# Optimization experiments

Measured on AMD Instinct MI355X. Metric: run time of the kernel, lower is better.

Reference implementation:

```python
import jax, jax.numpy as jnp
import numpy as np

B, T, C = 2, 2048, 1024
NH = 16
DFF = 4096
EPS = 1e-5


def setup_inputs() -> dict:
    key = jax.random.key(0)
    ks = jax.random.split(key, 12)
    s = 0.02
    return {
        "x": jax.random.normal(ks[0], (B, T, C), dtype=jnp.float32),
        "Wq": jax.random.normal(ks[1], (C, C), dtype=jnp.float32) * s,
        "bq": jax.random.normal(ks[2], (C,), dtype=jnp.float32) * s,
        "Wk": jax.random.normal(ks[3], (C, C), dtype=jnp.float32) * s,
        "bk": jax.random.normal(ks[4], (C,), dtype=jnp.float32) * s,
        "Wv": jax.random.normal(ks[5], (C, C), dtype=jnp.float32) * s,
        "bv": jax.random.normal(ks[6], (C,), dtype=jnp.float32) * s,
        "W1": jax.random.normal(ks[7], (C, DFF), dtype=jnp.float32) * s,
        "b1": jax.random.normal(ks[8], (DFF,), dtype=jnp.float32) * s,
        "W2": jax.random.normal(ks[9], (DFF, C), dtype=jnp.float32) * s,
        "b2": jax.random.normal(ks[10], (C,), dtype=jnp.float32) * s,
        "ln_w": jnp.ones((C,), dtype=jnp.float32),
    }


def _layernorm(x, w):
    # LayerNorm over last dim, weight only (bias=False), eps=1e-5
    mu = jnp.mean(x, axis=-1, keepdims=True)
    var = jnp.mean(jnp.square(x - mu), axis=-1, keepdims=True)
    return (x - mu) / jnp.sqrt(var + EPS) * w


def reference(x, Wq, bq, Wk, bk, Wv, bv, W1, b1, W2, b2, ln_w):
    Bx, Tx, Cx = x.shape
    hd = Cx // NH
    q = (x @ Wq + bq).reshape(Bx, Tx, NH, hd).transpose(0, 2, 1, 3)  # [B,H,T,hd]
    k = (x @ Wk + bk).reshape(Bx, Tx, NH, hd).transpose(0, 2, 1, 3)
    v = (x @ Wv + bv).reshape(Bx, Tx, NH, hd).transpose(0, 2, 1, 3)
    # NOTE: original scales by sqrt(d_k) = sqrt(FULL model dim C), not head dim
    scores = jnp.einsum("bhqd,bhkd->bhqk", q, k) / jnp.sqrt(jnp.float32(Cx))
    causal = jnp.tril(jnp.ones((Tx, Tx), dtype=bool))
    scores = jnp.where(causal[None, None, :, :], scores, -jnp.inf)
    attn = jax.nn.softmax(scores, axis=-1)
    head_out = jnp.einsum("bhqk,bhkd->bhqd", attn, v)
    a = head_out.transpose(0, 2, 1, 3).reshape(Bx, Tx, Cx)
    # residuals: out = x + ln(x) with SHARED ln weight
    h = a + _layernorm(a, ln_w)
    f = jax.nn.relu(h @ W1 + b1) @ W2 + b2
    out = f + _layernorm(f, ln_w)
    return out
```

## Files before the change

### kernel.cpp

```cpp
#include <hip/hip_runtime.h>
#include <math.h>


typedef __attribute__((ext_vector_type(8))) short short8;
typedef __attribute__((ext_vector_type(4))) float f32x4;

__device__ __forceinline__ unsigned short f2bf(float f) {
    unsigned u = __builtin_bit_cast(unsigned, f);
    unsigned r = u + 0x7fffu + ((u >> 16) & 1u);
    return (unsigned short)(r >> 16);
}

__global__ __launch_bounds__(256) void prep_kernel(
    const float* __restrict__ x,  const float* __restrict__ Wq,
    const float* __restrict__ Wk, const float* __restrict__ Wv,
    const float* __restrict__ W1, const float* __restrict__ W2,
    const float* __restrict__ bq, const float* __restrict__ bk,
    unsigned short* __restrict__ x_bf,  unsigned short* __restrict__ Wqk_t,
    unsigned short* __restrict__ Wvt,   unsigned short* __restrict__ W1t,
    unsigned short* __restrict__ W2t,   float* __restrict__ bqk)
{
    const int bid = blockIdx.x;
    const int tid = threadIdx.x;

    if (bid < 4096) {
        const int i = (bid * 256 + tid) * 4;
        float4 v = *(const float4*)(x + i);
        ushort4 o;
        o.x = f2bf(v.x); o.y = f2bf(v.y); o.z = f2bf(v.z); o.w = f2bf(v.w);
        *(ushort4*)(x_bf + i) = o;
        return;
    }
    if (bid >= 15360) {
        const int i = (bid - 15360) * 256 + tid;
        bqk[i] = i < 1024 ? bq[i] : bk[i - 1024];
        return;
    }

    __shared__ float tile[32][33];
    const float* src; unsigned short* dst; int K, N, t;
    if (bid < 5120)       { t = bid - 4096;  src = Wq; dst = Wqk_t;            K = 1024; N = 1024; }
    else if (bid < 6144)  { t = bid - 5120;  src = Wk; dst = Wqk_t + 1048576;  K = 1024; N = 1024; }
    else if (bid < 7168)  { t = bid - 6144;  src = Wv; dst = Wvt;              K = 1024; N = 1024; }
    else if (bid < 11264) { t = bid - 7168;  src = W1; dst = W1t;              K = 1024; N = 4096; }
    else                  { t = bid - 11264; src = W2; dst = W2t;              K = 4096; N = 1024; }

    const int ncols = N >> 5;
    const int n0 = (t % ncols) * 32;
    const int k0 = (t / ncols) * 32;
    const int tx = tid & 31;
    const int ty = tid >> 5;
#pragma unroll
    for (int i = 0; i < 4; ++i)
        tile[ty + i * 8][tx] = src[(size_t)(k0 + ty + i * 8) * N + n0 + tx];
    __syncthreads();
#pragma unroll
    for (int i = 0; i < 4; ++i)
        dst[(size_t)(n0 + ty + i * 8) * K + k0 + tx] = f2bf(tile[tx][ty + i * 8]);
}

template <int TM, int TN>
__device__ __forceinline__ void gemm_body(
    unsigned short* As, unsigned short* Bs,
    const unsigned short* __restrict__ A, const unsigned short* __restrict__ Bt,
    const float* __restrict__ bias, float* __restrict__ Cf,
    unsigned short* __restrict__ Cb, int M, int N, int K, int mode,
    int bx, int by)
{
    constexpr int NI   = TM / 32;
    constexpr int NJ   = TN / 32;
    constexpr int NPA  = TM / 8;
    constexpr int NPB  = TN / 8;
    constexpr int MAXA = (NPA + 3) / 4;
    constexpr int MAXB = (NPB + 3) / 4;

    const int tid  = threadIdx.x;
    const int lane = tid & 63;
    const int w    = tid >> 6;
    const int wm   = (w & 1) * (TM / 2);
    const int wn   = (w >> 1) * (TN / 2);
    const int fm   = lane & 15;
    const int quad = lane >> 4;

    const int row0 = by * TM;
    const int col0 = bx * TN;

    const int srow = lane >> 3;
    const int scol = ((lane & 7) ^ srow) << 3;

    const unsigned short* aptr[MAXA];
    int aoff[MAXA];
#pragma unroll
    for (int i = 0; i < MAXA; ++i) {
        const int p = w + i * 4;
        if (p < NPA) {
            aptr[i] = A + (size_t)(row0 + p * 8 + srow) * K + scol;
            aoff[i] = p * 8 * 64;
        }
    }
    const unsigned short* bptr[MAXB];
    int boff[MAXB];
#pragma unroll
    for (int i = 0; i < MAXB; ++i) {
        const int p = w + i * 4;
        if (p < NPB) {
            bptr[i] = Bt + (size_t)(col0 + p * 8 + srow) * K + scol;
            boff[i] = p * 8 * 64;
        }
    }

    f32x4 acc[NI][NJ] = {};

    for (int k0 = 0; k0 < K; k0 += 64) {
        __syncthreads();
#pragma unroll
        for (int i = 0; i < MAXA; ++i)
            if (w + i * 4 < NPA)
                __builtin_amdgcn_global_load_lds(
                    (const __attribute__((address_space(1))) void*)(aptr[i] + k0),
                    (__attribute__((address_space(3))) void*)&As[aoff[i]], 16, 0, 0);
#pragma unroll
        for (int i = 0; i < MAXB; ++i)
            if (w + i * 4 < NPB)
                __builtin_amdgcn_global_load_lds(
                    (const __attribute__((address_space(1))) void*)(bptr[i] + k0),
                    (__attribute__((address_space(3))) void*)&Bs[boff[i]], 16, 0, 0);
        __syncthreads();

#pragma unroll
        for (int kh = 0; kh < 2; ++kh) {
            short8 af[NI], bf[NJ];
#pragma unroll
            for (int i = 0; i < NI; ++i) {
                const int r = wm + i * 16 + fm;
                const int sl = ((kh << 2) | quad) ^ (r & 7);
                af[i] = *(const short8*)&As[r * 64 + sl * 8];
            }
#pragma unroll
            for (int j = 0; j < NJ; ++j) {
                const int r = wn + j * 16 + fm;
                const int sl = ((kh << 2) | quad) ^ (r & 7);
                bf[j] = *(const short8*)&Bs[r * 64 + sl * 8];
            }
#pragma unroll
            for (int i = 0; i < NI; ++i)
#pragma unroll
                for (int j = 0; j < NJ; ++j)
                    acc[i][j] = __builtin_amdgcn_mfma_f32_16x16x32_bf16(
                        af[i], bf[j], acc[i][j], 0, 0, 0);
        }
    }

#pragma unroll
    for (int j = 0; j < NJ; ++j) {
        const int col = col0 + wn + j * 16 + fm;
        const float bcol = (mode == 3) ? 0.f : bias[col];
#pragma unroll
        for (int i = 0; i < NI; ++i) {
            const int rbase = row0 + wm + i * 16 + quad * 4;
#pragma unroll
            for (int r = 0; r < 4; ++r) {
                const int row = rbase + r;
                float val = acc[i][j][r] + ((mode == 3) ? bias[row] : bcol);
                if (mode == 1) val = fmaxf(val, 0.f);
                if (mode == 0) Cf[(size_t)row * N + col] = val;
                else           Cb[(size_t)row * N + col] = f2bf(val);
            }
        }
    }
}

template <int TM, int TN>
__global__ __launch_bounds__(256) void gemm_bf16_mfma(
    const unsigned short* __restrict__ A, const unsigned short* __restrict__ Bt,
    const float* __restrict__ bias, float* __restrict__ Cf,
    unsigned short* __restrict__ Cb, int M, int N, int K, int mode)
{
    __shared__ unsigned short As[TM * 64];
    __shared__ unsigned short Bs[TN * 64];
    gemm_body<TM, TN>(As, Bs, A, Bt, bias, Cf, Cb, M, N, K, mode,
                      blockIdx.x, blockIdx.y);
}

template <int TM, int TN>
__global__ __launch_bounds__(256) void gemm_xcd(
    const unsigned short* __restrict__ A, const unsigned short* __restrict__ Bt,
    const float* __restrict__ bias, float* __restrict__ Cf,
    unsigned short* __restrict__ Cb, int M, int N, int K, int mode,
    int nx, int rows_per_xcd)
{
    __shared__ unsigned short As[TM * 64];
    __shared__ unsigned short Bs[TN * 64];
    const int xcd = blockIdx.x & 7;
    const int idx = blockIdx.x >> 3;
    const int bx  = idx % nx;
    const int by  = xcd * rows_per_xcd + idx / nx;
    gemm_body<TM, TN>(As, Bs, A, Bt, bias, Cf, Cb, M, N, K, mode, bx, by);
}

template <int TM, int TN>
__global__ __launch_bounds__(256) void gemm_dual(
    const unsigned short* __restrict__ A0, const unsigned short* __restrict__ B0,
    const float* __restrict__ bias0, unsigned short* __restrict__ C0,
    int M0, int N0, int K0, int mode0, int nb0, int nx0,
    const unsigned short* __restrict__ A1, const unsigned short* __restrict__ B1,
    const float* __restrict__ bias1, unsigned short* __restrict__ C1,
    int M1, int N1, int K1, int mode1, int nx1)
{
    __shared__ unsigned short As[TM * 64];
    __shared__ unsigned short Bs[TN * 64];
    const int bid = blockIdx.x;
    if (bid < nb0) {
        gemm_body<TM, TN>(As, Bs, A0, B0, bias0, nullptr, C0,
                          M0, N0, K0, mode0, bid % nx0, bid / nx0);
    } else {
        const int t = bid - nb0;
        gemm_body<TM, TN>(As, Bs, A1, B1, bias1, nullptr, C1,
                          M1, N1, K1, mode1, t % nx1, t / nx1);
    }
}

__global__ __launch_bounds__(256) void fattn_mfma(
    const unsigned short* __restrict__ qk,
    const unsigned short* __restrict__ vt,
    float* __restrict__ a)
{
    const int T = 2048, LDQK = 2048, LDVT = 4096, OUTC = 1024;
    const float cs = 0.04508422f;

    __shared__ unsigned short Qs[2][64][32];
    __shared__ unsigned short Ks[2][64][32];
    __shared__ unsigned short Vs[2][64][32];
    __shared__ unsigned short Ps[4][16][72];

    const int tid  = threadIdx.x;
    const int lane = tid & 63;
    const int w    = tid >> 6;
    const int fm   = lane & 15;
    const int quad = lane >> 4;
    const int srow = lane >> 2;
    const int scol = (lane & 3) * 8;

    const int n  = blockIdx.x;
    const int lo = n & 255, hi = n >> 8;
    const int h  = ((lo >> 5) & 7) | ((hi & 1) << 3);
    const int b  = hi >> 1;
    const int qv = lo & 31;
    const int u  = ((qv & 1) << 4) | ((qv & 2) << 2) | (qv & 4) |
                   ((qv & 8) >> 2) | ((qv & 16) >> 4);
    const int qb = (hi & 1) ? (31 - u) : u;
    const int q0 = qb * 64;

    const size_t rowbase = (size_t)b * T;

#pragma unroll
    for (int i = 0; i < 2; ++i) {
        const int c  = w * 2 + i;
        const int kh = c & 1, rg = c >> 1;
        const unsigned short* src = qk + (rowbase + q0 + rg * 16 + srow) * LDQK
                                       + h * 64 + kh * 32 + scol;
        __builtin_amdgcn_global_load_lds(
            (const __attribute__((address_space(1))) void*)src,
            (__attribute__((address_space(3))) void*)&Qs[kh][rg * 16][0], 16, 0, 0);
    }
    __syncthreads();
    short8 qf0 = *(const short8*)&Qs[0][w * 16 + fm][quad * 8];
    short8 qf1 = *(const short8*)&Qs[1][w * 16 + fm][quad * 8];

    short8 ones;
#pragma unroll
    for (int i = 0; i < 8; ++i) ones[i] = (short)0x3F80;

    f32x4 o[4] = {};
    f32x4 lacc = {};

    const int qglob = q0 + w * 16 + fm;

    for (int jt = 0; jt <= qb; ++jt) {
        const int j0 = jt * 64;
        __syncthreads();
#pragma unroll
        for (int i = 0; i < 2; ++i) {
            const int c  = w * 2 + i;
            const int kh = c & 1, rg = c >> 1;
            const unsigned short* ksrc = qk + (rowbase + j0 + rg * 16 + srow) * LDQK
                                            + 1024 + h * 64 + kh * 32 + scol;
            __builtin_amdgcn_global_load_lds(
                (const __attribute__((address_space(1))) void*)ksrc,
                (__attribute__((address_space(3))) void*)&Ks[kh][rg * 16][0], 16, 0, 0);
            const unsigned short* vsrc = vt + (size_t)(h * 64 + rg * 16 + srow) * LDVT
                                            + rowbase + j0 + kh * 32 + scol;
            __builtin_amdgcn_global_load_lds(
                (const __attribute__((address_space(1))) void*)vsrc,
                (__attribute__((address_space(3))) void*)&Vs[kh][rg * 16][0], 16, 0, 0);
        }
        __syncthreads();

        f32x4 s[4];
#pragma unroll
        for (int j = 0; j < 4; ++j) {
            short8 k0 = *(const short8*)&Ks[0][j * 16 + fm][quad * 8];
            short8 k1 = *(const short8*)&Ks[1][j * 16 + fm][quad * 8];
            f32x4 acc = {};
            acc = __builtin_amdgcn_mfma_f32_16x16x32_bf16(k0, qf0, acc, 0, 0, 0);
            acc = __builtin_amdgcn_mfma_f32_16x16x32_bf16(k1, qf1, acc, 0, 0, 0);
            s[j] = acc;
        }

        if (jt == qb) {
#pragma unroll
            for (int j = 0; j < 4; ++j) {
                const int kbase = j0 + j * 16 + quad * 4;
#pragma unroll
                for (int r = 0; r < 4; ++r) {
                    const float e = exp2f(s[j][r] * cs);
                    s[j][r] = (kbase + r > qglob) ? 0.f : e;
                }
            }
        } else {
#pragma unroll
            for (int j = 0; j < 4; ++j)
#pragma unroll
                for (int r = 0; r < 4; ++r)
                    s[j][r] = exp2f(s[j][r] * cs);
        }

#pragma unroll
        for (int j = 0; j < 4; ++j) {
            const unsigned d0 = (unsigned)f2bf(s[j][0]) | ((unsigned)f2bf(s[j][1]) << 16);
            const unsigned d1 = (unsigned)f2bf(s[j][2]) | ((unsigned)f2bf(s[j][3]) << 16);
            *(uint2*)&Ps[w][fm][j * 16 + quad * 4] = make_uint2(d0, d1);
        }
        short8 pf0 = *(const short8*)&Ps[w][fm][quad * 8];
        short8 pf1 = *(const short8*)&Ps[w][fm][32 + quad * 8];

#pragma unroll
        for (int jd = 0; jd < 4; ++jd) {
            short8 v0 = *(const short8*)&Vs[0][jd * 16 + fm][quad * 8];
            short8 v1 = *(const short8*)&Vs[1][jd * 16 + fm][quad * 8];
            o[jd] = __builtin_amdgcn_mfma_f32_16x16x32_bf16(pf0, v0, o[jd], 0, 0, 0);
            o[jd] = __builtin_amdgcn_mfma_f32_16x16x32_bf16(pf1, v1, o[jd], 0, 0, 0);
        }
        lacc = __builtin_amdgcn_mfma_f32_16x16x32_bf16(pf0, ones, lacc, 0, 0, 0);
        lacc = __builtin_amdgcn_mfma_f32_16x16x32_bf16(pf1, ones, lacc, 0, 0, 0);
    }

    const size_t orow = rowbase + q0 + w * 16 + quad * 4;
#pragma unroll
    for (int r = 0; r < 4; ++r) {
        const float inv = 1.0f / lacc[r];
#pragma unroll
        for (int jd = 0; jd < 4; ++jd)
            a[(orow + r) * OUTC + h * 64 + jd * 16 + fm] = o[jd][r] * inv;
    }
}

__global__ __launch_bounds__(256) void add_ln_kernel(
    const float* __restrict__ in, const float* __restrict__ w,
    float* __restrict__ outf, unsigned short* __restrict__ outb, int bf16_out)
{
    const int C = 1024;
    const int row = blockIdx.x;
    const int tid = threadIdx.x;

    __shared__ float red[256];

    const float* x = in + (size_t)row * C;
    float4 xv = *(const float4*)(x + tid * 4);

    red[tid] = xv.x + xv.y + xv.z + xv.w;
    __syncthreads();
    for (int off = 128; off > 0; off >>= 1) {
        if (tid < off) red[tid] += red[tid + off];
        __syncthreads();
    }
    const float mu = red[0] * (1.0f / 1024.0f);
    __syncthreads();

    float dx = xv.x - mu, dy = xv.y - mu, dz = xv.z - mu, dw = xv.w - mu;
    red[tid] = dx * dx + dy * dy + dz * dz + dw * dw;
    __syncthreads();
    for (int off = 128; off > 0; off >>= 1) {
        if (tid < off) red[tid] += red[tid + off];
        __syncthreads();
    }
    const float rstd = rsqrtf(red[0] * (1.0f / 1024.0f) + 1e-5f);

    float4 wv = *(const float4*)(w + tid * 4);
    float ox = xv.x + dx * rstd * wv.x;
    float oy = xv.y + dy * rstd * wv.y;
    float oz = xv.z + dz * rstd * wv.z;
    float ow = xv.w + dw * rstd * wv.w;
    if (bf16_out) {
        ushort4 o4;
        o4.x = f2bf(ox); o4.y = f2bf(oy); o4.z = f2bf(oz); o4.w = f2bf(ow);
        *(ushort4*)(outb + (size_t)row * C + tid * 4) = o4;
    } else {
        *(float4*)(outf + (size_t)row * C + tid * 4) = make_float4(ox, oy, oz, ow);
    }
}

extern "C" void kernel_launch(void* const* d_in, const int* in_sizes, int n_in,
                              void* d_out, int out_size, void* d_ws, size_t ws_size,
                              hipStream_t stream)
{
    const float* x    = (const float*)d_in[0];
    const float* Wq   = (const float*)d_in[1];
    const float* bq   = (const float*)d_in[2];
    const float* Wk   = (const float*)d_in[3];
    const float* bk   = (const float*)d_in[4];
    const float* Wv   = (const float*)d_in[5];
    const float* bv   = (const float*)d_in[6];
    const float* W1   = (const float*)d_in[7];
    const float* b1   = (const float*)d_in[8];
    const float* W2   = (const float*)d_in[9];
    const float* b2   = (const float*)d_in[10];
    const float* ln_w = (const float*)d_in[11];
    float* out = (float*)d_out;
    char* ws = (char*)d_ws;

    const int B = 2, T = 2048, C = 1024, DFF = 4096;
    const int M = B * T;
    const size_t MB = 1048576;

    unsigned short* qk_bf = (unsigned short*)(ws);
    unsigned short* vt_bf = (unsigned short*)(ws + 16 * MB);
    float*          a     = (float*)(ws + 24 * MB);
    unsigned short* x_bf  = (unsigned short*)(ws + 40 * MB);
    unsigned short* Wqk_t = (unsigned short*)(ws + 48 * MB);
    unsigned short* Wvt   = (unsigned short*)(ws + 52 * MB);
    unsigned short* W1t   = (unsigned short*)(ws + 54 * MB);
    unsigned short* W2t   = (unsigned short*)(ws + 62 * MB);
    float*          bqk   = (float*)(ws + 70 * MB);
    unsigned short* u_bf  = (unsigned short*)(ws + 71 * MB);
    unsigned short* h_bf  = x_bf;
    float*          f     = (float*)(ws);

    dim3 blk(256);

    prep_kernel<<<dim3(15368), blk, 0, stream>>>(
        x, Wq, Wk, Wv, W1, W2, bq, bk,
        x_bf, Wqk_t, Wvt, W1t, W2t, bqk);

    gemm_dual<64, 64><<<dim3(3072), blk, 0, stream>>>(
        x_bf, Wqk_t, bqk, qk_bf, M, 2 * C, C, 2, 2048, 32,
        Wvt, x_bf, bv, vt_bf, C, M, C, 3, 64);

    fattn_mfma<<<dim3(1024), blk, 0, stream>>>(qk_bf, vt_bf, a);

    add_ln_kernel<<<dim3(M), blk, 0, stream>>>(a, ln_w, nullptr, h_bf, 1);

    gemm_bf16_mfma<64, 128><<<dim3(DFF / 128, M / 64), blk, 0, stream>>>(
        h_bf, W1t, b1, nullptr, u_bf, M, DFF, C, 1);

    gemm_xcd<128, 64><<<dim3(512), blk, 0, stream>>>(
        u_bf, W2t, b2, f, nullptr, M, C, DFF, 0, 16, 4);

    add_ln_kernel<<<dim3(M), blk, 0, stream>>>(f, ln_w, out, nullptr, 0);
}
```

Before: 318.8 us.

## Enlarge GEMM tiles to 128x128 and split-K the down projection into two halves

Raises the QKV dual GEMM and the FFN up-projection GEMM to 128x128 tiles, so each block does more MFMA work per global load and fewer blocks are launched. The down projection switches to 128x128 tiles with a two-way split-K. Each half writes fp32 partial sums to a separate buffer, with the bias applied only in the first half, and the final add+layernorm kernel sums the two partials. This aims to raise data reuse while keeping enough blocks in flight for the down projection. The cost is an extra fp32 partial-output write and read, plus higher register and LDS use per block, which may lower occupancy.

```diff
diff --git a/kernel.cpp b/kernel.cpp
--- a/kernel.cpp
+++ b/kernel.cpp
@@ -65,7 +65,7 @@
     const unsigned short* __restrict__ A, const unsigned short* __restrict__ Bt,
     const float* __restrict__ bias, float* __restrict__ Cf,
     unsigned short* __restrict__ Cb, int M, int N, int K, int mode,
-    int bx, int by)
+    int bx, int by, int kbeg, int kend)
 {
     constexpr int NI   = TM / 32;
     constexpr int NJ   = TN / 32;
@@ -111,7 +111,7 @@
 
     f32x4 acc[NI][NJ] = {};
 
-    for (int k0 = 0; k0 < K; k0 += 64) {
+    for (int k0 = kbeg; k0 < kend; k0 += 64) {
         __syncthreads();
 #pragma unroll
         for (int i = 0; i < MAXA; ++i)
@@ -154,7 +154,7 @@
 #pragma unroll
     for (int j = 0; j < NJ; ++j) {
         const int col = col0 + wn + j * 16 + fm;
-        const float bcol = (mode == 3) ? 0.f : bias[col];
+        const float bcol = (mode == 3 || mode == 4) ? 0.f : bias[col];
 #pragma unroll
         for (int i = 0; i < NI; ++i) {
             const int rbase = row0 + wm + i * 16 + quad * 4;
@@ -163,8 +163,8 @@
                 const int row = rbase + r;
                 float val = acc[i][j][r] + ((mode == 3) ? bias[row] : bcol);
                 if (mode == 1) val = fmaxf(val, 0.f);
-                if (mode == 0) Cf[(size_t)row * N + col] = val;
-                else           Cb[(size_t)row * N + col] = f2bf(val);
+                if (mode == 0 || mode == 4) Cf[(size_t)row * N + col] = val;
+                else                        Cb[(size_t)row * N + col] = f2bf(val);
             }
         }
     }
@@ -179,23 +179,27 @@
     __shared__ unsigned short As[TM * 64];
     __shared__ unsigned short Bs[TN * 64];
     gemm_body<TM, TN>(As, Bs, A, Bt, bias, Cf, Cb, M, N, K, mode,
-                      blockIdx.x, blockIdx.y);
+                      blockIdx.x, blockIdx.y, 0, K);
 }
 
 template <int TM, int TN>
-__global__ __launch_bounds__(256) void gemm_xcd(
+__global__ __launch_bounds__(256) void gemm_splitk(
     const unsigned short* __restrict__ A, const unsigned short* __restrict__ Bt,
-    const float* __restrict__ bias, float* __restrict__ Cf,
-    unsigned short* __restrict__ Cb, int M, int N, int K, int mode,
-    int nx, int rows_per_xcd)
+    const float* __restrict__ bias, float* __restrict__ C0,
+    float* __restrict__ C1, int M, int N, int K,
+    int nxh, int rows_per_xcd_h, int nbh)
 {
     __shared__ unsigned short As[TM * 64];
     __shared__ unsigned short Bs[TN * 64];
-    const int xcd = blockIdx.x & 7;
-    const int idx = blockIdx.x >> 3;
-    const int bx  = idx % nx;
-    const int by  = xcd * rows_per_xcd + idx / nx;
-    gemm_body<TM, TN>(As, Bs, A, Bt, bias, Cf, Cb, M, N, K, mode, bx, by);
+    const int half = blockIdx.x >= nbh;
+    const int r    = blockIdx.x - (half ? nbh : 0);
+    const int xcd  = blockIdx.x & 7;
+    const int idx  = r >> 3;
+    const int bx   = idx % nxh;
+    const int by   = xcd * rows_per_xcd_h + idx / nxh;
+    const int kb   = half ? (K >> 1) : 0;
+    gemm_body<TM, TN>(As, Bs, A, Bt, bias, half ? C1 : C0, nullptr,
+                      M, N, K, half ? 4 : 0, bx, by, kb, kb + (K >> 1));
 }
 
 template <int TM, int TN>
@@ -212,11 +216,11 @@
     const int bid = blockIdx.x;
     if (bid < nb0) {
         gemm_body<TM, TN>(As, Bs, A0, B0, bias0, nullptr, C0,
-                          M0, N0, K0, mode0, bid % nx0, bid / nx0);
+                          M0, N0, K0, mode0, bid % nx0, bid / nx0, 0, K0);
     } else {
         const int t = bid - nb0;
         gemm_body<TM, TN>(As, Bs, A1, B1, bias1, nullptr, C1,
-                          M1, N1, K1, mode1, t % nx1, t / nx1);
+                          M1, N1, K1, mode1, t % nx1, t / nx1, 0, K1);
     }
 }
 
@@ -356,7 +360,8 @@
 }
 
 __global__ __launch_bounds__(256) void add_ln_kernel(
-    const float* __restrict__ in, const float* __restrict__ w,
+    const float* __restrict__ in, const float* __restrict__ in2,
+    const float* __restrict__ w,
     float* __restrict__ outf, unsigned short* __restrict__ outb, int bf16_out)
 {
     const int C = 1024;
@@ -367,6 +372,10 @@
 
     const float* x = in + (size_t)row * C;
     float4 xv = *(const float4*)(x + tid * 4);
+    if (in2) {
+        float4 yv = *(const float4*)(in2 + (size_t)row * C + tid * 4);
+        xv.x += yv.x; xv.y += yv.y; xv.z += yv.z; xv.w += yv.w;
+    }
 
     red[tid] = xv.x + xv.y + xv.z + xv.w;
     __syncthreads();
@@ -435,6 +444,7 @@
     unsigned short* u_bf  = (unsigned short*)(ws + 71 * MB);
     unsigned short* h_bf  = x_bf;
     float*          f     = (float*)(ws);
+    float*          f2    = a;
 
     dim3 blk(256);
 
@@ -442,19 +452,19 @@
         x, Wq, Wk, Wv, W1, W2, bq, bk,
         x_bf, Wqk_t, Wvt, W1t, W2t, bqk);
 
-    gemm_dual<64, 64><<<dim3(3072), blk, 0, stream>>>(
-        x_bf, Wqk_t, bqk, qk_bf, M, 2 * C, C, 2, 2048, 32,
-        Wvt, x_bf, bv, vt_bf, C, M, C, 3, 64);
+    gemm_dual<128, 128><<<dim3(768), blk, 0, stream>>>(
+        x_bf, Wqk_t, bqk, qk_bf, M, 2 * C, C, 2, 512, 16,
+        Wvt, x_bf, bv, vt_bf, C, M, C, 3, 32);
 
     fattn_mfma<<<dim3(1024), blk, 0, stream>>>(qk_bf, vt_bf, a);
 
-    add_ln_kernel<<<dim3(M), blk, 0, stream>>>(a, ln_w, nullptr, h_bf, 1);
-
-    gemm_bf16_mfma<64, 128><<<dim3(DFF / 128, M / 64), blk, 0, stream>>>(
+    add_ln_kernel<<<dim3(M), blk, 0, stream>>>(a, nullptr, ln_w, nullptr, h_bf, 1);
+
+    gemm_bf16_mfma<128, 128><<<dim3(DFF / 128, M / 128), blk, 0, stream>>>(
         h_bf, W1t, b1, nullptr, u_bf, M, DFF, C, 1);
 
-    gemm_xcd<128, 64><<<dim3(512), blk, 0, stream>>>(
-        u_bf, W2t, b2, f, nullptr, M, C, DFF, 0, 16, 4);
-
-    add_ln_kernel<<<dim3(M), blk, 0, stream>>>(f, ln_w, out, nullptr, 0);
-}
+    gemm_splitk<128, 128><<<dim3(512), blk, 0, stream>>>(
+        u_bf, W2t, b2, f, f2, M, C, DFF, 8, 4, 256);
+
+    add_ln_kernel<<<dim3(M), blk, 0, stream>>>(f, f2, ln_w, out, nullptr, 0);
+}
```

Result: slower. 335.2 us (+5.1%).
